# Performance work log

Measured on AMD Instinct MI355X. Metric: run time of the kernel, lower is better.

Reference implementation:

```python
import jax, jax.numpy as jnp
import numpy as np

B, S, HID = 2, 2048, 2048
NH, NKV, D = 32, 8, 64
M = 256          # FAVOR+ random features
CHUNK = 128      # causal chunk size
EPS = 1e-6


def setup_inputs():
    key = jax.random.key(0)
    ks = jax.random.split(key, 7)
    hidden_states = jax.random.normal(ks[0], (B, S, HID), jnp.float32)
    # RoPE tables (HF Llama style): [B, S, D]
    inv_freq = 1.0 / (10000.0 ** (jnp.arange(0, D, 2, dtype=jnp.float32) / D))
    freqs = jnp.arange(S, dtype=jnp.float32)[:, None] * inv_freq[None, :]   # [S, D/2]
    emb = jnp.concatenate([freqs, freqs], axis=-1)                          # [S, D]
    cos = jnp.broadcast_to(jnp.cos(emb)[None], (B, S, D)).astype(jnp.float32)
    sin = jnp.broadcast_to(jnp.sin(emb)[None], (B, S, D)).astype(jnp.float32)
    sc = 0.02
    Wq = jax.random.normal(ks[1], (NH * D, HID), jnp.float32) * sc
    Wk = jax.random.normal(ks[2], (NKV * D, HID), jnp.float32) * sc
    Wv = jax.random.normal(ks[3], (NKV * D, HID), jnp.float32) * sc
    Wo = jax.random.normal(ks[4], (HID, NH * D), jnp.float32) * sc
    proj = jax.random.normal(ks[5], (M, D), jnp.float32)  # FAVOR+ random projection
    return {"hidden_states": hidden_states, "cos": cos, "sin": sin,
            "Wq": Wq, "Wk": Wk, "Wv": Wv, "Wo": Wo, "proj": proj}


def rotate_half(x):
    x1, x2 = x[..., : x.shape[-1] // 2], x[..., x.shape[-1] // 2:]
    return jnp.concatenate([-x2, x1], axis=-1)


def favor_features(x, proj, is_query):
    # FAVOR+ positive softmax-kernel features: phi(x) = exp(Wx' - |x'|^2/2 - stab)/sqrt(m)
    dn = x.shape[-1] ** -0.25
    xn = x * dn                                            # data normalizer d^{-1/4}
    xp = jnp.einsum('bhsd,md->bhsm', xn, proj)             # [B,H,S,M]
    sq = 0.5 * jnp.sum(xn * xn, axis=-1, keepdims=True)
    if is_query:
        stab = jnp.max(xp, axis=-1, keepdims=True)
    else:
        stab = jnp.max(xp, axis=(-1, -2), keepdims=True)
    return (jnp.exp(xp - sq - stab) + EPS) / jnp.sqrt(jnp.asarray(M, xp.dtype))


def causal_linear_attention(phi_q, phi_k, v):
    # phi_q/phi_k: [B,H,S,M], v: [B,H,S,D]; causal chunked prefix formulation
    Bh, H, T, m = phi_q.shape
    d = v.shape[-1]
    nc = T // CHUNK
    qc = phi_q.reshape(Bh, H, nc, CHUNK, m)
    kc = phi_k.reshape(Bh, H, nc, CHUNK, m)
    vc = v.reshape(Bh, H, nc, CHUNK, d)
    # per-chunk KV state and key sums
    kv = jnp.einsum('bhscm,bhscd->bhsmd', kc, vc)          # [B,H,nc,M,D]
    kz = jnp.sum(kc, axis=3)                               # [B,H,nc,M]
    kv_pre = jnp.cumsum(kv, axis=2) - kv                   # exclusive prefix
    kz_pre = jnp.cumsum(kz, axis=2) - kz
    inter = jnp.einsum('bhscm,bhsmd->bhscd', qc, kv_pre)
    inter_z = jnp.einsum('bhscm,bhsm->bhsc', qc, kz_pre)
    # intra-chunk causal part
    mask = jnp.tril(jnp.ones((CHUNK, CHUNK), phi_q.dtype))
    scores = jnp.einsum('bhscm,bhstm->bhsct', qc, kc) * mask
    intra = jnp.einsum('bhsct,bhstd->bhscd', scores, vc)
    intra_z = jnp.sum(scores, axis=-1)
    out = (inter + intra) / (inter_z + intra_z + EPS)[..., None]
    return out.reshape(Bh, H, T, d)


def reference(hidden_states, cos, sin, Wq, Wk, Wv, Wo, proj):
    b, s, _ = hidden_states.shape
    q = (hidden_states @ Wq.T).reshape(b, s, NH, D).transpose(0, 2, 1, 3)   # [B,NH,S,D]
    k = (hidden_states @ Wk.T).reshape(b, s, NKV, D).transpose(0, 2, 1, 3)  # [B,NKV,S,D]
    v = (hidden_states @ Wv.T).reshape(b, s, NKV, D).transpose(0, 2, 1, 3)
    c, si = cos[:, None, :, :], sin[:, None, :, :]
    q = q * c + rotate_half(q) * si
    k = k * c + rotate_half(k) * si
    groups = NH // NKV
    k = jnp.repeat(k, groups, axis=1)
    v = jnp.repeat(v, groups, axis=1)
    phi_q = favor_features(q, proj, is_query=True)
    phi_k = favor_features(k, proj, is_query=False)
    attn = causal_linear_attention(phi_q, phi_k, v)                         # [B,NH,S,D]
    attn = attn.transpose(0, 2, 1, 3).reshape(b, s, NH * D)
    return attn @ Wo.T
```

## Files before the change

kernel.cpp:

```cpp
#include <hip/hip_runtime.h>
#include <hip/hip_bf16.h>

#define SEQ   2048
#define NHEAD 32
#define NKVH  8
#define DH    64
#define MFEAT 256
#define NCH   16
#define EPSF  1e-6f

typedef __hip_bfloat16 bf16;
typedef unsigned short u16;
typedef __attribute__((ext_vector_type(8))) short short8;
typedef __attribute__((ext_vector_type(4))) float f32x4;

__device__ __forceinline__ float b2f(bf16 x){ return __bfloat162float(x); }
__device__ __forceinline__ bf16  f2b(float x){ return __float2bfloat16(x); }
__device__ __forceinline__ u16   f2u(float x){ bf16 h = __float2bfloat16(x); return *reinterpret_cast<u16*>(&h); }

__device__ __forceinline__ bool probe_f32(const unsigned* __restrict__ p){
  return (p[0] & 0xFFFFu) == 0u;
}
__device__ __forceinline__ float loadIn(const void* __restrict__ ptr, size_t idx, bool f32){
  return f32 ? ((const float*)ptr)[idx] : b2f(((const bf16*)ptr)[idx]);
}

__device__ __forceinline__ void cp16(u16* lds, const u16* g){
  __builtin_amdgcn_global_load_lds((const __attribute__((address_space(1))) unsigned*)g,
      (__attribute__((address_space(3))) unsigned*)lds, 16, 0, 0);
}

#define MFMA16(a,b,c) __builtin_amdgcn_mfma_f32_16x16x32_bf16(a,b,c,0,0,0)
#define SBAR()  do { __builtin_amdgcn_s_barrier(); __builtin_amdgcn_sched_barrier(0); } while(0)

__global__ __launch_bounds__(256) void conv_kernel(const void* __restrict__ src,
    u16* __restrict__ dst, const unsigned* __restrict__ probe)
{
  const bool f32in = probe_f32(probe);
  size_t i = (size_t)blockIdx.x*256 + threadIdx.x;
  if (f32in){
    const float4* s = (const float4*)src;
    float4 a = s[i*2], b = s[i*2+1];
    u16 t[8] = {f2u(a.x),f2u(a.y),f2u(a.z),f2u(a.w),
                f2u(b.x),f2u(b.y),f2u(b.z),f2u(b.w)};
    *(short8*)&dst[i*8] = *(const short8*)t;
  } else {
    ((short8*)dst)[i] = ((const short8*)src)[i];
  }
}

__global__ __launch_bounds__(512) void gemm_mfma(const u16* __restrict__ A,
    const u16* __restrict__ W, float* __restrict__ oq, float* __restrict__ ok,
    float* __restrict__ ov, void* __restrict__ outAny, int K, int N, int mode,
    const void* __restrict__ cosg, const void* __restrict__ sing,
    const unsigned* __restrict__ probe)
{
  __shared__ __align__(16) u16 sA[3][16384];
  __shared__ __align__(16) u16 sB[3][8192];
  const int tid = threadIdx.x;
  const int lane = tid & 63, wave = tid >> 6;

  const int nbx = gridDim.x;
  const int nwg = nbx * gridDim.y;
  int id = blockIdx.y * nbx + blockIdx.x;
  int sw = id;
  if ((nwg & 7) == 0) sw = (id & 7) * (nwg >> 3) + (id >> 3);
  const int bx = sw % nbx, by = sw / nbx;
  const int c0 = bx*128, r0 = by*256;

  const int wm = wave >> 1, wn = wave & 1;
  f32x4 acc[4][4] = {};

  const int rl  = lane >> 3;
  const int swzE = ((lane & 7) ^ rl) << 3;
  const u16* gA = A + (size_t)(r0 + wave*8 + rl)*K + swzE;
  const u16* gB = W + (size_t)(c0 + wave*8 + rl)*K + swzE;
  const int aDst = wave*512;
  const int bDst = wave*512;

  const int rowA = (wm*64 + (lane&15))*64;
  const int rowB = (wn*64 + (lane&15))*64;
  const int colS = (((lane>>4)*8) ^ ((lane&7)<<3));

  const int nk = K >> 6;

  #define STAGE_ALL(buf, t) do { const int k0_ = (t)*64;                  \
    cp16(&sA[buf][aDst],         gA + k0_);                               \
    cp16(&sA[buf][aDst + 4096],  gA + (size_t)64*K  + k0_);               \
    cp16(&sA[buf][aDst + 8192],  gA + (size_t)128*K + k0_);               \
    cp16(&sA[buf][aDst + 12288], gA + (size_t)192*K + k0_);               \
    cp16(&sB[buf][bDst],         gB + k0_);                               \
    cp16(&sB[buf][bDst + 4096],  gB + (size_t)64*K  + k0_); } while(0)

  STAGE_ALL(0, 0);
  STAGE_ALL(1, 1);

  int cur = 0;
  for (int t = 0; t < nk; ++t) {
    if (t < nk-1) asm volatile("s_waitcnt vmcnt(6)" ::: "memory");
    else          asm volatile("s_waitcnt vmcnt(0)" ::: "memory");
    SBAR();

    int sb = cur + 2; if (sb >= 3) sb -= 3;
    const int k0s = (t + 2) * 64;
    const bool st = (t + 2 < nk);
    const u16* bA_ = sA[cur];
    const u16* bB_ = sB[cur];

    short8 a01[2][2], a23[2][2], b01[2][2], b23[2][2];

    #pragma unroll
    for (int mt=0;mt<2;++mt){
      a01[mt][0] = *(const short8*)(bA_ + rowA + mt*1024 + colS);
      a01[mt][1] = *(const short8*)(bA_ + rowA + mt*1024 + (colS^32));
    }
    #pragma unroll
    for (int nt=0;nt<2;++nt){
      b01[nt][0] = *(const short8*)(bB_ + rowB + nt*1024 + colS);
      b01[nt][1] = *(const short8*)(bB_ + rowB + nt*1024 + (colS^32));
    }
    if (st){ cp16(&sA[sb][aDst], gA + k0s);
             cp16(&sA[sb][aDst + 4096], gA + (size_t)64*K + k0s); }
    SBAR();
    __builtin_amdgcn_s_setprio(1);
    #pragma unroll
    for (int mt=0;mt<2;++mt)
      #pragma unroll
      for (int nt=0;nt<2;++nt){
        acc[mt][nt] = MFMA16(a01[mt][0], b01[nt][0], acc[mt][nt]);
        acc[mt][nt] = MFMA16(a01[mt][1], b01[nt][1], acc[mt][nt]);
      }
    __builtin_amdgcn_s_setprio(0);
    SBAR();

    #pragma unroll
    for (int nt=0;nt<2;++nt){
      b23[nt][0] = *(const short8*)(bB_ + rowB + (nt+2)*1024 + colS);
      b23[nt][1] = *(const short8*)(bB_ + rowB + (nt+2)*1024 + (colS^32));
    }
    if (st){ cp16(&sA[sb][aDst + 8192],  gA + (size_t)128*K + k0s);
             cp16(&sA[sb][aDst + 12288], gA + (size_t)192*K + k0s); }
    SBAR();
    __builtin_amdgcn_s_setprio(1);
    #pragma unroll
    for (int mt=0;mt<2;++mt)
      #pragma unroll
      for (int nt=0;nt<2;++nt){
        acc[mt][nt+2] = MFMA16(a01[mt][0], b23[nt][0], acc[mt][nt+2]);
        acc[mt][nt+2] = MFMA16(a01[mt][1], b23[nt][1], acc[mt][nt+2]);
      }
    __builtin_amdgcn_s_setprio(0);
    SBAR();

    #pragma unroll
    for (int mt=0;mt<2;++mt){
      a23[mt][0] = *(const short8*)(bA_ + rowA + (mt+2)*1024 + colS);
      a23[mt][1] = *(const short8*)(bA_ + rowA + (mt+2)*1024 + (colS^32));
    }
    if (st){ cp16(&sB[sb][bDst], gB + k0s);
             cp16(&sB[sb][bDst + 4096], gB + (size_t)64*K + k0s); }
    SBAR();
    __builtin_amdgcn_s_setprio(1);
    #pragma unroll
    for (int mt=0;mt<2;++mt)
      #pragma unroll
      for (int nt=0;nt<2;++nt){
        acc[mt+2][nt+2] = MFMA16(a23[mt][0], b23[nt][0], acc[mt+2][nt+2]);
        acc[mt+2][nt+2] = MFMA16(a23[mt][1], b23[nt][1], acc[mt+2][nt+2]);
      }
    __builtin_amdgcn_s_setprio(0);
    SBAR();

    __builtin_amdgcn_s_setprio(1);
    #pragma unroll
    for (int mt=0;mt<2;++mt)
      #pragma unroll
      for (int nt=0;nt<2;++nt){
        acc[mt+2][nt] = MFMA16(a23[mt][0], b01[nt][0], acc[mt+2][nt]);
        acc[mt+2][nt] = MFMA16(a23[mt][1], b01[nt][1], acc[mt+2][nt]);
      }
    __builtin_amdgcn_s_setprio(0);

    cur = (cur == 2) ? 0 : cur + 1;
  }
  #undef STAGE_ALL

  const int rbase = r0 + wm*64 + (lane>>4)*4;
  const int cbase = c0 + wn*64 + (lane&15);
  if (mode == 0) {
    const bool f32o = probe_f32(probe);
    #pragma unroll
    for (int mt=0;mt<4;++mt)
      #pragma unroll
      for (int nt=0;nt<4;++nt)
        #pragma unroll
        for (int rg=0;rg<4;++rg){
          int r = rbase + mt*16 + rg, c = cbase + nt*16;
          float v = acc[mt][nt][rg];
          if (f32o) ((float*)outAny)[(size_t)r*N + c] = v;
          else      ((u16*)outAny)[(size_t)r*N + c] = f2u(v);
        }
  } else {
    const bool f32in = probe_f32(probe);
    const float dn = 0.3535533905932738f;
    #pragma unroll
    for (int nt=0;nt<4;++nt){
      int cc = cbase + nt*16;
      float* dst; int H2, cl; bool isv = false;
      if (cc < 2048){ dst = oq; H2 = 32; cl = cc; }
      else if (cc < 2560){ dst = ok; H2 = 8; cl = cc - 2048; }
      else { dst = ov; H2 = 8; cl = cc - 2560; isv = true; }
      int hh = cl>>6, dd = cl&63;
      float sgn = (dd < 32) ? -1.f : 1.f;
      #pragma unroll
      for (int mt=0;mt<4;++mt)
        #pragma unroll
        for (int rg=0;rg<4;++rg){
          int r = rbase + mt*16 + rg;
          int bb = r>>11, s = r&2047;
          float v = acc[mt][nt][rg];
          if (!isv){
            float vp = acc[mt][nt^2][rg];
            size_t ci = ((size_t)bb*SEQ + s)*DH + dd;
            float cv = loadIn(cosg, ci, f32in);
            float sv = loadIn(sing, ci, f32in);
            v = (v*cv + sgn*vp*sv) * dn;
          }
          dst[(((size_t)bb*H2 + hh)*SEQ + s)*DH + dd] = v;
        }
    }
  }
}

__global__ __launch_bounds__(256) void phi_mfma(const float* __restrict__ xn,
    const u16* __restrict__ projb, float* __restrict__ rmaxk,
    const float* __restrict__ stabk, u16* __restrict__ phi, int mode)
{
  __shared__ __align__(16) u16 sA[64*80];
  __shared__ __align__(16) u16 sP[256*80];
  __shared__ float sq[64];
  const int tid = threadIdx.x, lane = tid & 63, wave = tid >> 6;
  const size_t row0 = (size_t)blockIdx.x * 64;

  #pragma unroll
  for (int l = 0; l < 8; ++l){
    int v8 = tid + l*256;
    int off = v8*8; int m = off>>6, d = off&63;
    *(short8*)&sP[m*80 + d] = ((const short8*)projb)[v8];
  }
  {
    int r = tid >> 2, qq = tid & 3;
    const float* src = xn + (row0 + r)*DH + qq*16;
    float s = 0.f;
    u16 tmp[16];
    #pragma unroll
    for (int i=0;i<16;i+=4){
      float4 v4 = *(const float4*)&src[i];
      s += v4.x*v4.x + v4.y*v4.y + v4.z*v4.z + v4.w*v4.w;
      tmp[i] = f2u(v4.x); tmp[i+1] = f2u(v4.y); tmp[i+2] = f2u(v4.z); tmp[i+3] = f2u(v4.w);
    }
    *(short8*)&sA[r*80 + qq*16]     = *(short8*)&tmp[0];
    *(short8*)&sA[r*80 + qq*16 + 8] = *(short8*)&tmp[8];
    s += __shfl_xor(s, 1, 64);
    s += __shfl_xor(s, 2, 64);
    if (qq == 0) sq[r] = 0.5f*s;
  }
  __syncthreads();

  f32x4 acc[16] = {};
  const u16* pA = &sA[(wave*16 + (lane&15))*80 + (lane>>4)*8];
  short8 af0 = *(const short8*)(pA);
  short8 af1 = *(const short8*)(pA + 32);
  #pragma unroll
  for (int nt=0; nt<16; ++nt){
    const u16* pB = &sP[(nt*16 + (lane&15))*80 + (lane>>4)*8];
    short8 b0 = *(const short8*)(pB);
    short8 b1 = *(const short8*)(pB + 32);
    acc[nt] = MFMA16(af0, b0, acc[nt]);
    acc[nt] = MFMA16(af1, b1, acc[nt]);
  }

  float mx[4];
  #pragma unroll
  for (int rg=0; rg<4; ++rg){
    float m = acc[0][rg];
    #pragma unroll
    for (int nt=1; nt<16; ++nt) m = fmaxf(m, acc[nt][rg]);
    m = fmaxf(m, __shfl_xor(m, 1, 64));
    m = fmaxf(m, __shfl_xor(m, 2, 64));
    m = fmaxf(m, __shfl_xor(m, 4, 64));
    m = fmaxf(m, __shfl_xor(m, 8, 64));
    mx[rg] = m;
  }
  const int rloc = wave*16 + (lane>>4)*4;
  if (mode == 1){
    if ((lane & 15) == 0){
      #pragma unroll
      for (int rg=0;rg<4;++rg) rmaxk[row0 + rloc + rg] = mx[rg];
    }
    return;
  }
  float stab[4];
  if (mode == 0){
    #pragma unroll
    for (int rg=0;rg<4;++rg) stab[rg] = mx[rg];
  } else {
    float s = stabk[row0 >> 11];
    #pragma unroll
    for (int rg=0;rg<4;++rg) stab[rg] = s;
  }
  float sqr[4];
  #pragma unroll
  for (int rg=0;rg<4;++rg) sqr[rg] = sq[rloc + rg];
  #pragma unroll
  for (int nt=0;nt<16;++nt){
    #pragma unroll
    for (int rg=0;rg<4;++rg){
      float val = (__expf(fminf(acc[nt][rg] - sqr[rg] - stab[rg], 0.f)) + EPSF) * 0.0625f;
      phi[(row0 + rloc + rg)*MFEAT + nt*16 + (lane&15)] = f2u(val);
    }
  }
}

__global__ void stab_reduce_kernel(const float* __restrict__ rmaxk, float* __restrict__ stabk){
  __shared__ float red[256];
  int bk = blockIdx.x;
  float mx = -1e30f;
  for (int i = threadIdx.x; i < SEQ; i += 256) mx = fmaxf(mx, rmaxk[(size_t)bk*SEQ + i]);
  red[threadIdx.x] = mx; __syncthreads();
  for (int off=128; off>0; off>>=1){
    if ((int)threadIdx.x < off) red[threadIdx.x] = fmaxf(red[threadIdx.x], red[threadIdx.x+off]);
    __syncthreads();
  }
  if (threadIdx.x==0) stabk[bk] = red[0];
}

__global__ __launch_bounds__(256) void kvchunk_kernel(const bf16* __restrict__ phik,
    const float* __restrict__ vbuf, float* __restrict__ kv, float* __restrict__ kz)
{
  int blk = blockIdx.x; int bk = blk >> 4, c = blk & 15;
  const bf16* Kc = phik + ((size_t)bk*SEQ + c*128)*MFEAT;
  const float* Vc = vbuf + ((size_t)bk*SEQ + c*128)*DH;
  __shared__ float sV[128*64];
  for (int l=0;l<32;++l){ int idx = threadIdx.x + l*256; sV[idx] = Vc[idx]; }
  __syncthreads();
  int m = threadIdx.x;
  float acc[64] = {}; float az = 0.f;
  for (int t=0;t<128;++t){
    float ph = b2f(Kc[(size_t)t*MFEAT + m]);
    az += ph;
    const float4* vr = (const float4*)&sV[t*64];
    #pragma unroll
    for (int d4=0; d4<16; ++d4){
      float4 v4 = vr[d4];
      acc[d4*4+0] += ph*v4.x; acc[d4*4+1] += ph*v4.y;
      acc[d4*4+2] += ph*v4.z; acc[d4*4+3] += ph*v4.w;
    }
  }
  float* out = kv + (size_t)blk*MFEAT*DH + (size_t)m*DH;
  #pragma unroll
  for (int d4=0; d4<16; ++d4)
    ((float4*)out)[d4] = make_float4(acc[d4*4],acc[d4*4+1],acc[d4*4+2],acc[d4*4+3]);
  kz[(size_t)blk*MFEAT + m] = az;
}

__global__ void scan_kernel(float* __restrict__ p, int inner, int nc, int total){
  int t = blockIdx.x*256 + threadIdx.x;
  if (t >= total) return;
  int outer = t / inner, rem = t - outer*inner;
  float* base = p + (size_t)outer*nc*inner + rem;
  float run = 0.f;
  for (int c=0;c<nc;++c){
    float v = base[(size_t)c*inner];
    base[(size_t)c*inner] = run;
    run += v;
  }
}

__global__ __launch_bounds__(256) void attn_mfma(
    const u16* __restrict__ phiq, const u16* __restrict__ phik,
    const float* __restrict__ vbuf, const float* __restrict__ kvp,
    const float* __restrict__ kzp, u16* __restrict__ attnout)
{
  __shared__ __align__(16) u16 smem[28288];
  __shared__ float sZ[128];
  const int tid = threadIdx.x, lane = tid & 63, wave = tid >> 6;
  const int blk = blockIdx.x;
  const int c = blk & 15, h = (blk >> 4) & 31, b = blk >> 9;
  const int kvh = h >> 2;
  const u16* Q   = phiq + (((size_t)(b*NHEAD+h)*SEQ) + c*128)*MFEAT;
  const u16* Kc  = phik + (((size_t)(b*NKVH+kvh)*SEQ) + c*128)*MFEAT;
  const float* Vc  = vbuf + (((size_t)(b*NKVH+kvh)*SEQ) + c*128)*DH;
  const float* KVp = kvp + ((size_t)((b*NKVH+kvh)*NCH + c))*MFEAT*DH;
  const float* KZp = kzp + ((size_t)((b*NKVH+kvh)*NCH + c))*MFEAT;

  u16* sQ   = smem;
  u16* sK   = smem + 4096;
  u16* sKVT = smem + 8192;
  u16* sP   = smem;
  u16* sVT  = smem + 17408;

  f32x4 accS[2][8] = {};
  f32x4 accO[2][5] = {};

  const int ch0 = wave*64 + lane, ch1 = 256 + wave*64 + lane;
  const u16* gQ0 = Q  + (ch0>>2)*MFEAT + (ch0&3)*8;
  const u16* gQ1 = Q  + (ch1>>2)*MFEAT + (ch1&3)*8;
  const u16* gK0 = Kc + (ch0>>2)*MFEAT + (ch0&3)*8;
  const u16* gK1 = Kc + (ch1>>2)*MFEAT + (ch1&3)*8;
  u16* lQ0 = &sQ[(wave*64)*8];  u16* lQ1 = &sQ[(256+wave*64)*8];
  u16* lK0 = &sK[(wave*64)*8];  u16* lK1 = &sK[(256+wave*64)*8];

  for (int k0 = 0; k0 < MFEAT; k0 += 32) {
    cp16(lQ0, gQ0 + k0); cp16(lQ1, gQ1 + k0);
    cp16(lK0, gK0 + k0); cp16(lK1, gK1 + k0);
    #pragma unroll
    for (int i=0;i<8;++i){
      int idx = tid + i*256;
      int m = idx >> 6, d = idx & 63;
      int col = (((m>>3) ^ ((d>>3)&3))<<3) | (m&7);
      sKVT[d*72 + col] = f2u(KVp[(size_t)(k0+m)*DH + d]);
    }
    if (tid < 32) sKVT[64*72 + tid] = f2u(KZp[k0 + tid]);
    __syncthreads();
    short8 af0, af1;
    const u16* pQ = &sQ[(wave*32 + (lane&15))*32 + (lane>>4)*8];
    af0 = *(const short8*)(pQ);
    af1 = *(const short8*)(pQ + 512);
    #pragma unroll
    for (int nt=0;nt<8;++nt){
      short8 bk = *(const short8*)&sK[(nt*16 + (lane&15))*32 + (lane>>4)*8];
      accS[0][nt] = MFMA16(af0, bk, accS[0][nt]);
      accS[1][nt] = MFMA16(af1, bk, accS[1][nt]);
    }
    #pragma unroll
    for (int nt=0;nt<5;++nt){
      int row = nt*16 + (lane&15);
      int g   = ((lane>>4) ^ ((row>>3)&3)) << 3;
      short8 bi = *(const short8*)&sKVT[row*72 + g];
      accO[0][nt] = MFMA16(af0, bi, accO[0][nt]);
      accO[1][nt] = MFMA16(af1, bi, accO[1][nt]);
    }
    __syncthreads();
  }

  #pragma unroll
  for (int mt=0;mt<2;++mt){
    int rowb = wave*32 + mt*16 + (lane>>4)*4;
    #pragma unroll
    for (int nt=0;nt<8;++nt){
      int col = nt*16 + (lane&15);
      #pragma unroll
      for (int rg=0;rg<4;++rg){
        int row = rowb + rg;
        float v = (col <= row) ? accS[mt][nt][rg] : 0.f;
        sP[row*136 + col] = f2u(v);
      }
    }
  }
  #pragma unroll
  for (int i=0;i<32;++i){
    int idx = tid + i*256;
    int t = idx >> 6, d = idx & 63;
    sVT[d*136 + t] = f2u(Vc[idx]);
  }
  if (tid < 128) sVT[64*136 + tid] = 0x3F80;
  __syncthreads();

  #pragma unroll
  for (int kc=0;kc<4;++kc){
    const u16* pP = &sP[(wave*32 + (lane&15))*136 + kc*32 + (lane>>4)*8];
    short8 pa0 = *(const short8*)(pP);
    short8 pa1 = *(const short8*)(pP + 16*136);
    #pragma unroll
    for (int nt=0;nt<5;++nt){
      short8 bv = *(const short8*)&sVT[(nt*16 + (lane&15))*136 + kc*32 + (lane>>4)*8];
      accO[0][nt] = MFMA16(pa0, bv, accO[0][nt]);
      accO[1][nt] = MFMA16(pa1, bv, accO[1][nt]);
    }
  }

  if ((lane & 15) == 0){
    #pragma unroll
    for (int mt=0;mt<2;++mt){
      int rowb = wave*32 + mt*16 + (lane>>4)*4;
      #pragma unroll
      for (int rg=0;rg<4;++rg) sZ[rowb + rg] = accO[mt][4][rg];
    }
  }
  __syncthreads();
  const int d0 = lane & 15;
  #pragma unroll
  for (int mt=0;mt<2;++mt){
    int rowb = wave*32 + mt*16 + (lane>>4)*4;
    #pragma unroll
    for (int rg=0;rg<4;++rg){
      int row = rowb + rg;
      float inv = 1.0f / (sZ[row] + EPSF);
      int sg = c*128 + row;
      size_t ob = (((size_t)b*SEQ + sg)*NHEAD + h)*DH;
      #pragma unroll
      for (int nt=0;nt<4;++nt)
        attnout[ob + nt*16 + d0] = f2u(accO[mt][nt][rg] * inv);
    }
  }
}

extern "C" void kernel_launch(void* const* d_in, const int* in_sizes, int n_in,
                              void* d_out, int out_size, void* d_ws, size_t ws_size,
                              hipStream_t stream)
{
  const void* hidden = d_in[0];
  const void* cosg   = d_in[1];
  const void* sing   = d_in[2];
  const void* Wq     = d_in[3];
  const void* Wk     = d_in[4];
  const void* Wv     = d_in[5];
  const void* Wo     = d_in[6];
  const void* proj   = d_in[7];
  const unsigned* probe = (const unsigned*)d_in[1];

  float* ws = (float*)d_ws;
  float* xnq   = ws;
  float* kv    = ws;
  float* kz    = ws + 4194304;
  float* rmaxk = ws + 4259840;
  float* stabk = ws + 4292608;
  float* xnk   = ws + 8388608;
  float* vbuf  = ws + 10485760;
  u16*   projb = (u16*) (ws + 12582912);
  bf16*  phiq  = (bf16*)(ws + 12591104);
  bf16*  phik  = (bf16*)(ws + 29368320);
  u16*   hb    = (u16*) (ws + 33562624);
  u16*   attn  = (u16*) (ws + 33562624);
  u16*   wqkv  = (u16*) (ws + 37756928);
  u16*   wob   = (u16*) (ws + 37756928);

  conv_kernel<<<4096, 256, 0, stream>>>(hidden, hb, probe);
  conv_kernel<<<2048, 256, 0, stream>>>(Wq, wqkv,           probe);
  conv_kernel<<<512,  256, 0, stream>>>(Wk, wqkv + 4194304, probe);
  conv_kernel<<<512,  256, 0, stream>>>(Wv, wqkv + 5242880, probe);
  conv_kernel<<<8,    256, 0, stream>>>(proj, projb, probe);

  gemm_mfma<<<dim3(24,16), 512, 0, stream>>>(hb, wqkv, xnq, xnk, vbuf, nullptr,
                                             2048, 3072, 1, cosg, sing, probe);
  conv_kernel<<<2048, 256, 0, stream>>>(Wo, wob, probe);

  phi_mfma<<<2048, 256, 0, stream>>>(xnq, projb, nullptr, nullptr, (u16*)phiq, 0);
  phi_mfma<<<512,  256, 0, stream>>>(xnk, projb, rmaxk, nullptr, nullptr, 1);
  stab_reduce_kernel<<<16, 256, 0, stream>>>(rmaxk, stabk);
  phi_mfma<<<512,  256, 0, stream>>>(xnk, projb, nullptr, stabk, (u16*)phik, 2);

  kvchunk_kernel<<<256, 256, 0, stream>>>(phik, vbuf, kv, kz);
  scan_kernel<<<1024, 256, 0, stream>>>(kv, MFEAT*DH, NCH, 16*MFEAT*DH);
  scan_kernel<<<16,   256, 0, stream>>>(kz, MFEAT,    NCH, 16*MFEAT);

  attn_mfma<<<1024, 256, 0, stream>>>((const u16*)phiq, (const u16*)phik,
                                      vbuf, kv, kz, attn);

  gemm_mfma<<<dim3(16,16), 512, 0, stream>>>(attn, wob, nullptr, nullptr, nullptr,
                                             d_out, 2048, 2048, 0, nullptr, nullptr, probe);
}
```

Baseline: 446.8 us.

## Precompute bf16 transposed V and KV prefix states for async loads in attention

A new kernel transposes V into a bf16 [bkv, D, S] layout. kvchunk now writes KV state transposed, and the scan emits bf16 prefix sums. attn_mfma can then copy V^T, KV^T and Z straight into swizzled shared memory with cp16, instead of doing scalar fp32 loads, conversions and scattered LDS stores inside its loop. The cost is an extra kernel launch and extra workspace traffic, and kvchunk now issues strided uncoalesced stores.

```diff
diff --git a/kernel.cpp b/kernel.cpp
--- a/kernel.cpp
+++ b/kernel.cpp
@@ -335,6 +335,26 @@
   if (threadIdx.x==0) stabk[bk] = red[0];
 }
 
+__global__ __launch_bounds__(256) void vtrans_kernel(const float* __restrict__ vbuf,
+                                                     u16* __restrict__ vT)
+{
+  int blk = blockIdx.x;
+  int bk = blk >> 4, sc = blk & 15;
+  const float* src = vbuf + ((size_t)bk*SEQ + sc*128)*DH;
+  __shared__ float sT[128*65];
+  for (int i=0;i<32;++i){ int idx = threadIdx.x + i*256; sT[(idx>>6)*65 + (idx&63)] = src[idx]; }
+  __syncthreads();
+  #pragma unroll
+  for (int i=0;i<4;++i){
+    int gi = threadIdx.x + i*256;
+    int d = gi >> 4, t8 = (gi & 15)*8;
+    u16 tmp[8];
+    #pragma unroll
+    for (int j=0;j<8;++j) tmp[j] = f2u(sT[(t8+j)*65 + d]);
+    *(short8*)&vT[((size_t)bk*DH + d)*SEQ + sc*128 + t8] = *(const short8*)tmp;
+  }
+}
+
 __global__ __launch_bounds__(256) void kvchunk_kernel(const bf16* __restrict__ phik,
     const float* __restrict__ vbuf, float* __restrict__ kv, float* __restrict__ kz)
 {
@@ -357,42 +377,44 @@
       acc[d4*4+2] += ph*v4.z; acc[d4*4+3] += ph*v4.w;
     }
   }
-  float* out = kv + (size_t)blk*MFEAT*DH + (size_t)m*DH;
-  #pragma unroll
-  for (int d4=0; d4<16; ++d4)
-    ((float4*)out)[d4] = make_float4(acc[d4*4],acc[d4*4+1],acc[d4*4+2],acc[d4*4+3]);
+  float* out = kv + (size_t)blk*MFEAT*DH;
+  #pragma unroll
+  for (int d=0; d<64; ++d) out[(size_t)d*MFEAT + m] = acc[d];
   kz[(size_t)blk*MFEAT + m] = az;
 }
 
-__global__ void scan_kernel(float* __restrict__ p, int inner, int nc, int total){
+__global__ void scan_kernel(float* __restrict__ p, u16* __restrict__ ob,
+                            int inner, int nc, int total){
   int t = blockIdx.x*256 + threadIdx.x;
   if (t >= total) return;
   int outer = t / inner, rem = t - outer*inner;
-  float* base = p + (size_t)outer*nc*inner + rem;
+  const float* base = p + (size_t)outer*nc*inner + rem;
+  u16* obase = ob + (size_t)outer*nc*inner + rem;
   float run = 0.f;
   for (int c=0;c<nc;++c){
     float v = base[(size_t)c*inner];
-    base[(size_t)c*inner] = run;
+    obase[(size_t)c*inner] = f2u(run);
     run += v;
   }
 }
 
 __global__ __launch_bounds__(256) void attn_mfma(
     const u16* __restrict__ phiq, const u16* __restrict__ phik,
-    const float* __restrict__ vbuf, const float* __restrict__ kvp,
-    const float* __restrict__ kzp, u16* __restrict__ attnout)
-{
-  __shared__ __align__(16) u16 smem[28288];
+    const u16* __restrict__ kvpb, const u16* __restrict__ kzpb,
+    const u16* __restrict__ vT, u16* __restrict__ attnout)
+{
+  __shared__ __align__(16) u16 smem[27648];
   __shared__ float sZ[128];
   const int tid = threadIdx.x, lane = tid & 63, wave = tid >> 6;
   const int blk = blockIdx.x;
   const int c = blk & 15, h = (blk >> 4) & 31, b = blk >> 9;
   const int kvh = h >> 2;
+  const int bkv = b*NKVH + kvh;
   const u16* Q   = phiq + (((size_t)(b*NHEAD+h)*SEQ) + c*128)*MFEAT;
-  const u16* Kc  = phik + (((size_t)(b*NKVH+kvh)*SEQ) + c*128)*MFEAT;
-  const float* Vc  = vbuf + (((size_t)(b*NKVH+kvh)*SEQ) + c*128)*DH;
-  const float* KVp = kvp + ((size_t)((b*NKVH+kvh)*NCH + c))*MFEAT*DH;
-  const float* KZp = kzp + ((size_t)((b*NKVH+kvh)*NCH + c))*MFEAT;
+  const u16* Kc  = phik + (((size_t)bkv*SEQ) + c*128)*MFEAT;
+  const u16* KVb = kvpb + ((size_t)(bkv*NCH + c))*MFEAT*DH;
+  const u16* KZb = kzpb + ((size_t)(bkv*NCH + c))*MFEAT;
+  const u16* vTb = vT + (size_t)bkv*DH*SEQ;
 
   u16* sQ   = smem;
   u16* sK   = smem + 4096;
@@ -402,6 +424,14 @@
 
   f32x4 accS[2][8] = {};
   f32x4 accO[2][5] = {};
+
+  #pragma unroll
+  for (int i=0;i<4;++i){
+    int gi = tid + i*256;
+    int d  = gi >> 4, g = gi & 15;
+    cp16(&sVT[(i*256 + wave*64)*8],
+         vTb + (size_t)d*SEQ + c*128 + ((g ^ (d&7))<<3));
+  }
 
   const int ch0 = wave*64 + lane, ch1 = 256 + wave*64 + lane;
   const u16* gQ0 = Q  + (ch0>>2)*MFEAT + (ch0&3)*8;
@@ -411,17 +441,14 @@
   u16* lQ0 = &sQ[(wave*64)*8];  u16* lQ1 = &sQ[(256+wave*64)*8];
   u16* lK0 = &sK[(wave*64)*8];  u16* lK1 = &sK[(256+wave*64)*8];
 
+  const int dKV = wave*16 + (lane>>2);
+  const u16* gKVsrc = KVb + (size_t)dKV*MFEAT + (((lane&3) ^ (dKV&3))<<3);
+
   for (int k0 = 0; k0 < MFEAT; k0 += 32) {
     cp16(lQ0, gQ0 + k0); cp16(lQ1, gQ1 + k0);
     cp16(lK0, gK0 + k0); cp16(lK1, gK1 + k0);
-    #pragma unroll
-    for (int i=0;i<8;++i){
-      int idx = tid + i*256;
-      int m = idx >> 6, d = idx & 63;
-      int col = (((m>>3) ^ ((d>>3)&3))<<3) | (m&7);
-      sKVT[d*72 + col] = f2u(KVp[(size_t)(k0+m)*DH + d]);
-    }
-    if (tid < 32) sKVT[64*72 + tid] = f2u(KZp[k0 + tid]);
+    cp16(&sKVT[wave*512], gKVsrc + k0);
+    if (tid < 4) cp16(&sKVT[2048], KZb + k0 + tid*8);
     __syncthreads();
     short8 af0, af1;
     const u16* pQ = &sQ[(wave*32 + (lane&15))*32 + (lane>>4)*8];
@@ -436,8 +463,7 @@
     #pragma unroll
     for (int nt=0;nt<5;++nt){
       int row = nt*16 + (lane&15);
-      int g   = ((lane>>4) ^ ((row>>3)&3)) << 3;
-      short8 bi = *(const short8*)&sKVT[row*72 + g];
+      short8 bi = *(const short8*)&sKVT[row*32 + (((lane>>4) ^ (row&3))<<3)];
       accO[0][nt] = MFMA16(af0, bi, accO[0][nt]);
       accO[1][nt] = MFMA16(af1, bi, accO[1][nt]);
     }
@@ -458,13 +484,10 @@
       }
     }
   }
-  #pragma unroll
-  for (int i=0;i<32;++i){
-    int idx = tid + i*256;
-    int t = idx >> 6, d = idx & 63;
-    sVT[d*136 + t] = f2u(Vc[idx]);
-  }
-  if (tid < 128) sVT[64*136 + tid] = 0x3F80;
+  if (tid < 16){
+    u16 ones[8] = {0x3F80,0x3F80,0x3F80,0x3F80,0x3F80,0x3F80,0x3F80,0x3F80};
+    *(short8*)&sVT[64*128 + tid*8] = *(const short8*)ones;
+  }
   __syncthreads();
 
   #pragma unroll
@@ -474,7 +497,9 @@
     short8 pa1 = *(const short8*)(pP + 16*136);
     #pragma unroll
     for (int nt=0;nt<5;++nt){
-      short8 bv = *(const short8*)&sVT[(nt*16 + (lane&15))*136 + kc*32 + (lane>>4)*8];
+      int row = nt*16 + (lane&15);
+      int g   = kc*4 + (lane>>4);
+      short8 bv = *(const short8*)&sVT[row*128 + ((g ^ (row&7))<<3)];
       accO[0][nt] = MFMA16(pa0, bv, accO[0][nt]);
       accO[1][nt] = MFMA16(pa1, bv, accO[1][nt]);
     }
@@ -526,6 +551,9 @@
   float* kz    = ws + 4194304;
   float* rmaxk = ws + 4259840;
   float* stabk = ws + 4292608;
+  u16*   vT    = (u16*) (ws + 4292864);
+  u16*   kvpb  = (u16*) (ws + 5341440);
+  u16*   kzpb  = (u16*) (ws + 7438592);
   float* xnk   = ws + 8388608;
   float* vbuf  = ws + 10485760;
   u16*   projb = (u16*) (ws + 12582912);
@@ -547,16 +575,17 @@
   conv_kernel<<<2048, 256, 0, stream>>>(Wo, wob, probe);
 
   phi_mfma<<<2048, 256, 0, stream>>>(xnq, projb, nullptr, nullptr, (u16*)phiq, 0);
+  vtrans_kernel<<<256, 256, 0, stream>>>(vbuf, vT);
   phi_mfma<<<512,  256, 0, stream>>>(xnk, projb, rmaxk, nullptr, nullptr, 1);
   stab_reduce_kernel<<<16, 256, 0, stream>>>(rmaxk, stabk);
   phi_mfma<<<512,  256, 0, stream>>>(xnk, projb, nullptr, stabk, (u16*)phik, 2);
 
   kvchunk_kernel<<<256, 256, 0, stream>>>(phik, vbuf, kv, kz);
-  scan_kernel<<<1024, 256, 0, stream>>>(kv, MFEAT*DH, NCH, 16*MFEAT*DH);
-  scan_kernel<<<16,   256, 0, stream>>>(kz, MFEAT,    NCH, 16*MFEAT);
+  scan_kernel<<<1024, 256, 0, stream>>>(kv, kvpb, MFEAT*DH, NCH, 16*MFEAT*DH);
+  scan_kernel<<<16,   256, 0, stream>>>(kz, kzpb, MFEAT,    NCH, 16*MFEAT);
 
   attn_mfma<<<1024, 256, 0, stream>>>((const u16*)phiq, (const u16*)phik,
-                                      vbuf, kv, kz, attn);
+                                      kvpb, kzpb, vT, attn);
 
   gemm_mfma<<<dim3(16,16), 512, 0, stream>>>(attn, wob, nullptr, nullptr, nullptr,
                                              d_out, 2048, 2048, 0, nullptr, nullptr, probe);
```

Result: no change. 441.7 us (-1.2%).
